# Kernel optimization log

Hardware: AMD Instinct MI355X
Metric: run time of the kernel (lower is better)

## Reference

```python
import jax, jax.numpy as jnp
import numpy as np

N_HEADS = 32
N_KV_HEADS = 8
HEAD_DIM = 128


def setup_inputs() -> dict:
    key = jax.random.key(0)
    ks = jax.random.split(key, 7)
    B, S, D = 2, 2048, 4096
    scale = 0.02
    x = jax.random.normal(ks[0], (B, S, D), dtype=jnp.float32)
    wq = jax.random.normal(ks[1], (D, D), dtype=jnp.float32) * scale
    wk = jax.random.normal(ks[2], (N_KV_HEADS * HEAD_DIM, D), dtype=jnp.float32) * scale
    wv = jax.random.normal(ks[3], (N_KV_HEADS * HEAD_DIM, D), dtype=jnp.float32) * scale
    wo = jax.random.normal(ks[4], (D, D), dtype=jnp.float32) * scale
    # RoPE frequencies: theta = 10000^{-2i/d}, angles = pos * theta
    inv_freq = 1.0 / (10000.0 ** (jnp.arange(0, HEAD_DIM, 2, dtype=jnp.float32) / HEAD_DIM))
    angles = jnp.arange(S, dtype=jnp.float32)[:, None] * inv_freq[None, :]  # (S, HEAD_DIM//2)
    freqs_cos = jnp.cos(angles)
    freqs_sin = jnp.sin(angles)
    # causal additive mask (0 on/below diagonal, -inf above)
    neg_inf = jnp.finfo(jnp.float32).min
    mask = jnp.where(jnp.triu(jnp.ones((S, S), dtype=bool), k=1), neg_inf, 0.0)[None, None]
    return {"x": x, "wq": wq, "wk": wk, "wv": wv, "wo": wo,
            "freqs_cos": freqs_cos, "freqs_sin": freqs_sin, "mask": mask,
            "start_pos": 0}


def _apply_rope(t, cos, sin):
    # t: (B, S, H, D); cos/sin: (S, D//2) -> broadcast (1, S, 1, D//2)
    b, s, h, d = t.shape
    tr = t.reshape(b, s, h, d // 2, 2)
    te, to = tr[..., 0], tr[..., 1]
    c = cos[None, :, None, :]
    si = sin[None, :, None, :]
    out = jnp.stack([te * c - to * si, te * si + to * c], axis=-1)
    return out.reshape(b, s, h, d)


def reference(x, wq, wk, wv, wo, freqs_cos, freqs_sin, mask, start_pos):
    b, s, d = x.shape
    n_rep = N_HEADS // N_KV_HEADS
    xq = (x @ wq.T).reshape(b, s, N_HEADS, HEAD_DIM)
    xk = (x @ wk.T).reshape(b, s, N_KV_HEADS, HEAD_DIM)
    xv = (x @ wv.T).reshape(b, s, N_KV_HEADS, HEAD_DIM)
    xq = _apply_rope(xq, freqs_cos, freqs_sin)
    xk = _apply_rope(xk, freqs_cos, freqs_sin)
    # repeat_kv: (B, S, Hkv, D) -> (B, S, Hkv*n_rep, D)
    keys = jnp.broadcast_to(xk[:, :, :, None, :], (b, s, N_KV_HEADS, n_rep, HEAD_DIM)).reshape(b, s, N_HEADS, HEAD_DIM)
    values = jnp.broadcast_to(xv[:, :, :, None, :], (b, s, N_KV_HEADS, n_rep, HEAD_DIM)).reshape(b, s, N_HEADS, HEAD_DIM)
    q = xq.transpose(0, 2, 1, 3)       # (B, H, S, D)
    k = keys.transpose(0, 2, 1, 3)
    v = values.transpose(0, 2, 1, 3)
    scores = jnp.einsum("bhqd,bhkd->bhqk", q, k) / np.sqrt(HEAD_DIM).astype(np.float32)
    scores = scores + mask
    probs = jax.nn.softmax(scores.astype(jnp.float32), axis=-1).astype(q.dtype)
    out = jnp.einsum("bhqk,bhkd->bhqd", probs, v)
    out = out.transpose(0, 2, 1, 3).reshape(b, s, N_HEADS * HEAD_DIM)
    return out @ wo.T
```

## Files before the change

### kernel.cpp

```cpp
#include <hip/hip_runtime.h>
#include <cstdint>
#include <cstddef>

#define B_  2
#define S_  2048
#define D_  4096
#define NH  32
#define NKV 8
#define HD  128

typedef unsigned short u16;
typedef unsigned int   u32;
typedef __attribute__((ext_vector_type(8))) short short8;
typedef __attribute__((ext_vector_type(4))) float f32x4;

__device__ __forceinline__ u16 f2bf(float f) {
  u32 u = __float_as_uint(f);
  u32 r = (u + 0x7FFFu + ((u >> 16) & 1u)) >> 16;
  return (u16)r;
}
__device__ __forceinline__ float bf2f(u32 lo16) {
  return __uint_as_float(lo16 << 16);
}
__device__ __forceinline__ u32 cvtpk_bf16(float lo, float hi) {
  u32 r;
  asm("v_cvt_pk_bf16_f32 %0, %1, %2" : "=v"(r) : "v"(lo), "v"(hi));
  return r;
}
__device__ __forceinline__ void load_lds16(const void* g, void* lds) {
  __builtin_amdgcn_global_load_lds(
      (const __attribute__((address_space(1))) u32*)g,
      (__attribute__((address_space(3))) u32*)lds, 16, 0, 0);
}

__global__ __launch_bounds__(256) void cvt_all(
    const float* __restrict__ x, const float* __restrict__ wq,
    const float* __restrict__ wk, const float* __restrict__ wv,
    const float* __restrict__ wo, u16* __restrict__ Xb, u16* __restrict__ Wqb,
    u16* __restrict__ Wkb, u16* __restrict__ Wvb, u16* __restrict__ Wob) {
  long i = (long)blockIdx.x * 256 + threadIdx.x;
  const float* src; u16* dst; long off;
  if (i < 2097152L)      { src = x;  dst = Xb;  off = i; }
  else if (i < 4194304L) { src = wq; dst = Wqb; off = i - 2097152L; }
  else if (i < 4718592L) { src = wk; dst = Wkb; off = i - 4194304L; }
  else if (i < 5242880L) { src = wv; dst = Wvb; off = i - 4718592L; }
  else                   { src = wo; dst = Wob; off = i - 5242880L; }
  const float4* s = (const float4*)src + off * 2;
  float4 a = s[0], b = s[1];
  uint4 o;
  o.x = (u32)f2bf(a.x) | ((u32)f2bf(a.y) << 16);
  o.y = (u32)f2bf(a.z) | ((u32)f2bf(a.w) << 16);
  o.z = (u32)f2bf(b.x) | ((u32)f2bf(b.y) << 16);
  o.w = (u32)f2bf(b.z) | ((u32)f2bf(b.w) << 16);
  *((uint4*)dst + off) = o;
}

template <int MODE, bool ROPE>
__global__ __launch_bounds__(512, 2)
void gemm256(const u16* __restrict__ A, const u16* __restrict__ Bw,
             void* __restrict__ Cout, int M, int N, int K, int Hh,
             const float* __restrict__ fc, const float* __restrict__ fs) {
  const int tid = threadIdx.x, lid = tid & 63, w = tid >> 6;
  const int lr = lid & 15, lg = lid >> 4;
  const int wm = w >> 2, wn = w & 3;

  int lin = blockIdx.y * gridDim.x + blockIdx.x;
  int bm, bn;
  if (gridDim.x == 16 && gridDim.y == 16) {
    int xcd = lin & 7, idx = lin >> 3;
    bm = ((xcd & 3) * 4 + (idx >> 3)) * 256;
    bn = ((xcd >> 2) * 8 + (idx & 7)) * 256;
  } else {
    bm = blockIdx.y * 256;
    bn = blockIdx.x * 256;
  }

  __shared__ __align__(16) u16 Al[2][2][8192];
  __shared__ __align__(16) u16 Bl[2][2][8192];

  f32x4 acc[8][4];
#pragma unroll
  for (int i = 0; i < 8; ++i)
#pragma unroll
    for (int j = 0; j < 4; ++j) acc[i][j] = (f32x4){0.f, 0.f, 0.f, 0.f};

#define STG_A(B2, KS, K0)                                                       \
  do {                                                                          \
    _Pragma("unroll")                                                           \
    for (int j_ = 0; j_ < 2; ++j_) {                                            \
      int c_ = j_ * 512 + tid;                                                  \
      int r_ = c_ >> 2, cb_ = c_ & 3;                                           \
      int s_ = (cb_ ^ (r_ >> 1)) & 3;                                           \
      load_lds16(A + (size_t)(bm + r_) * K + (K0) + (KS) * 32 + s_ * 8,         \
                 &Al[B2][KS][c_ * 8]);                                          \
    }                                                                           \
  } while (0)
#define STG_B(B2, KS, K0)                                                       \
  do {                                                                          \
    _Pragma("unroll")                                                           \
    for (int j_ = 0; j_ < 2; ++j_) {                                            \
      int c_ = j_ * 512 + tid;                                                  \
      int r_ = c_ >> 2, cb_ = c_ & 3;                                           \
      int s_ = (cb_ ^ (r_ >> 1)) & 3;                                           \
      load_lds16(Bw + (size_t)(bn + r_) * K + (K0) + (KS) * 32 + s_ * 8,        \
                 &Bl[B2][KS][c_ * 8]);                                          \
    }                                                                           \
  } while (0)

  const int nt = K >> 6;
  STG_A(0, 0, 0); STG_B(0, 0, 0); STG_A(0, 1, 0); STG_B(0, 1, 0);
  STG_A(1, 0, 64); STG_B(1, 0, 64);
  asm volatile("s_waitcnt vmcnt(8)" ::: "memory");
  __builtin_amdgcn_s_barrier();

  for (int t = 0; t < nt; ++t) {
    const int buf = t & 1, bufN = buf ^ 1;
    const int k1 = (t + 1) << 6, k2 = (t + 2) << 6;
    const bool pf1 = (t + 1 < nt), pf2 = (t + 2 < nt);
    short8 a[4], bfr[4];

#pragma unroll
    for (int ni = 0; ni < 4; ++ni) {
      int r = wn * 64 + ni * 16 + lr;
      bfr[ni] = *(const short8*)&Bl[buf][0][r * 32 + ((lg ^ (r >> 1)) & 3) * 8];
    }
#pragma unroll
    for (int mi = 0; mi < 4; ++mi) {
      int r = wm * 128 + mi * 16 + lr;
      a[mi] = *(const short8*)&Al[buf][0][r * 32 + ((lg ^ (r >> 1)) & 3) * 8];
    }
    if (pf1) STG_A(bufN, 1, k1);
    __builtin_amdgcn_s_barrier();
    __builtin_amdgcn_s_setprio(1);
#pragma unroll
    for (int mi = 0; mi < 4; ++mi)
#pragma unroll
      for (int ni = 0; ni < 4; ++ni)
        acc[mi][ni] = __builtin_amdgcn_mfma_f32_16x16x32_bf16(a[mi], bfr[ni], acc[mi][ni], 0, 0, 0);
    __builtin_amdgcn_s_setprio(0);

#pragma unroll
    for (int mi = 0; mi < 4; ++mi) {
      int r = wm * 128 + (mi + 4) * 16 + lr;
      a[mi] = *(const short8*)&Al[buf][0][r * 32 + ((lg ^ (r >> 1)) & 3) * 8];
    }
    if (pf1) STG_B(bufN, 1, k1);
    __builtin_amdgcn_s_barrier();
    __builtin_amdgcn_s_setprio(1);
#pragma unroll
    for (int mi = 0; mi < 4; ++mi)
#pragma unroll
      for (int ni = 0; ni < 4; ++ni)
        acc[mi + 4][ni] = __builtin_amdgcn_mfma_f32_16x16x32_bf16(a[mi], bfr[ni], acc[mi + 4][ni], 0, 0, 0);
    __builtin_amdgcn_s_setprio(0);

    if (pf1) asm volatile("s_waitcnt vmcnt(8)" ::: "memory");
    else     asm volatile("s_waitcnt vmcnt(0)" ::: "memory");
    __builtin_amdgcn_s_barrier();

#pragma unroll
    for (int ni = 0; ni < 4; ++ni) {
      int r = wn * 64 + ni * 16 + lr;
      bfr[ni] = *(const short8*)&Bl[buf][1][r * 32 + ((lg ^ (r >> 1)) & 3) * 8];
    }
#pragma unroll
    for (int mi = 0; mi < 4; ++mi) {
      int r = wm * 128 + mi * 16 + lr;
      a[mi] = *(const short8*)&Al[buf][1][r * 32 + ((lg ^ (r >> 1)) & 3) * 8];
    }
    if (pf2) STG_A(buf, 0, k2);
    __builtin_amdgcn_s_barrier();
    __builtin_amdgcn_s_setprio(1);
#pragma unroll
    for (int mi = 0; mi < 4; ++mi)
#pragma unroll
      for (int ni = 0; ni < 4; ++ni)
        acc[mi][ni] = __builtin_amdgcn_mfma_f32_16x16x32_bf16(a[mi], bfr[ni], acc[mi][ni], 0, 0, 0);
    __builtin_amdgcn_s_setprio(0);

#pragma unroll
    for (int mi = 0; mi < 4; ++mi) {
      int r = wm * 128 + (mi + 4) * 16 + lr;
      a[mi] = *(const short8*)&Al[buf][1][r * 32 + ((lg ^ (r >> 1)) & 3) * 8];
    }
    if (pf2) STG_B(buf, 0, k2);
    __builtin_amdgcn_s_barrier();
    __builtin_amdgcn_s_setprio(1);
#pragma unroll
    for (int mi = 0; mi < 4; ++mi)
#pragma unroll
      for (int ni = 0; ni < 4; ++ni)
        acc[mi + 4][ni] = __builtin_amdgcn_mfma_f32_16x16x32_bf16(a[mi], bfr[ni], acc[mi + 4][ni], 0, 0, 0);
    __builtin_amdgcn_s_setprio(0);

    if (pf1) {
      if (pf2) asm volatile("s_waitcnt vmcnt(8)" ::: "memory");
      else     asm volatile("s_waitcnt vmcnt(4)" ::: "memory");
      __builtin_amdgcn_s_barrier();
    }
  }
#undef STG_A
#undef STG_B

#pragma unroll
  for (int mi = 0; mi < 8; ++mi)
#pragma unroll
    for (int ni = 0; ni < 4; ++ni)
#pragma unroll
      for (int v = 0; v < 4; ++v) {
        int m = bm + wm * 128 + mi * 16 + lg * 4 + v;
        int n = bn + wn * 64 + ni * 16 + lr;
        float val = acc[mi][ni][v];
        if (ROPE) {
          int srow = m & (S_ - 1);
          int j = (n & (HD - 1)) >> 1;
          float c = fc[(size_t)srow * 64 + j];
          float s = fs[(size_t)srow * 64 + j];
          float partner = __shfl_xor(val, 1);
          val = (n & 1) ? (val * c + partner * s) : (val * c - partner * s);
        }
        if (MODE == 0) {
          ((float*)Cout)[(size_t)m * N + n] = val;
        } else if (MODE == 1) {
          int b = m >> 11, s = m & (S_ - 1), hh = n >> 7, d = n & (HD - 1);
          ((u16*)Cout)[(((size_t)(b * Hh + hh)) * S_ + s) * HD + d] = f2bf(val);
        } else {
          int b = m >> 11, s = m & (S_ - 1), hh = n >> 7, d = n & (HD - 1);
          ((u16*)Cout)[(((size_t)(b * Hh + hh)) * HD + d) * S_ + s] = f2bf(val);
        }
      }
}

__global__ __launch_bounds__(256)
void gemm_kv(const u16* __restrict__ Xb, const u16* __restrict__ Wk,
             const u16* __restrict__ Wv, u16* __restrict__ Kr, u16* __restrict__ Vt,
             const float* __restrict__ fc, const float* __restrict__ fs) {
  const int tid = threadIdx.x;
  const int lid = tid & 63, w = tid >> 6;
  const int lr = lid & 15, lg = lid >> 4;
  const int wm = w >> 1, wn = w & 1;
  const int zz = blockIdx.z;
  const u16* Bw = zz ? Wv : Wk;
  const int K = D_, N = NKV * HD;

  const int gx = gridDim.x;
  const int nwg = gx * gridDim.y;
  const int lin = blockIdx.y * gx + blockIdx.x;
  const int cpx = nwg >> 3;
  const int lin2 = (lin & 7) * cpx + (lin >> 3);
  const int bm = (lin2 / gx) * 128, bn = (lin2 % gx) * 128;

  __shared__ __align__(16) u16 Al[128 * 64];
  __shared__ __align__(16) u16 Bl[128 * 64];
  f32x4 acc[4][4];
#pragma unroll
  for (int i = 0; i < 4; ++i)
#pragma unroll
    for (int j = 0; j < 4; ++j) acc[i][j] = (f32x4){0.f, 0.f, 0.f, 0.f};

  for (int k0 = 0; k0 < K; k0 += 64) {
    __syncthreads();
#pragma unroll
    for (int i = 0; i < 4; ++i) {
      int c = i * 256 + tid;
      int row = c >> 3, cb = c & 7;
      int cbs = (cb ^ row) & 7;
      load_lds16(Xb + (size_t)(bm + row) * K + k0 + cbs * 8, &Al[c * 8]);
    }
#pragma unroll
    for (int i = 0; i < 4; ++i) {
      int c = i * 256 + tid;
      int row = c >> 3, cb = c & 7;
      int cbs = (cb ^ row) & 7;
      load_lds16(Bw + (size_t)(bn + row) * K + k0 + cbs * 8, &Bl[c * 8]);
    }
    __syncthreads();
#pragma unroll
    for (int ks = 0; ks < 2; ++ks) {
      short8 af[4], bf[4];
#pragma unroll
      for (int mi = 0; mi < 4; ++mi) {
        int row = wm * 64 + mi * 16 + lr;
        af[mi] = *(const short8*)&Al[row * 64 + (((ks * 4 + lg) ^ row) & 7) * 8];
      }
#pragma unroll
      for (int ni = 0; ni < 4; ++ni) {
        int row = wn * 64 + ni * 16 + lr;
        bf[ni] = *(const short8*)&Bl[row * 64 + (((ks * 4 + lg) ^ row) & 7) * 8];
      }
#pragma unroll
      for (int mi = 0; mi < 4; ++mi)
#pragma unroll
        for (int ni = 0; ni < 4; ++ni)
          acc[mi][ni] = __builtin_amdgcn_mfma_f32_16x16x32_bf16(af[mi], bf[ni], acc[mi][ni], 0, 0, 0);
    }
  }
#pragma unroll
  for (int mi = 0; mi < 4; ++mi)
#pragma unroll
    for (int ni = 0; ni < 4; ++ni)
#pragma unroll
      for (int v = 0; v < 4; ++v) {
        int m = bm + wm * 64 + mi * 16 + lg * 4 + v;
        int n = bn + wn * 64 + ni * 16 + lr;
        float val = acc[mi][ni][v];
        int b = m >> 11, s = m & (S_ - 1), hh = n >> 7, d = n & (HD - 1);
        if (zz == 0) {
          int j = d >> 1;
          float c = fc[(size_t)s * 64 + j];
          float sn = fs[(size_t)s * 64 + j];
          float partner = __shfl_xor(val, 1);
          val = (n & 1) ? (val * c + partner * sn) : (val * c - partner * sn);
          Kr[(((size_t)(b * NKV + hh)) * S_ + s) * HD + d] = f2bf(val);
        } else {
          Vt[(((size_t)(b * NKV + hh)) * HD + d) * S_ + s] = f2bf(val);
        }
      }
}

__global__ __launch_bounds__(512, 4)
void attn_k(const u16* __restrict__ Qr, const u16* __restrict__ Kr,
            const u16* __restrict__ Vt, u16* __restrict__ Ao) {
  const int xp = blockIdx.x, h = blockIdx.y, b = blockIdx.z;
  const int kvh = h >> 2;
  const int tid = threadIdx.x, lid = tid & 63, w = tid >> 6;
  const int lr = lid & 15, lg = lid >> 4;
  __shared__ __align__(16) u16 Kl[2][64 * 128];
  __shared__ __align__(16) u16 Vl[2][128 * 64];
  __shared__ __align__(16) u32 Plw[8 * 512];

  const size_t qbase = ((size_t)(b * NH + h)) * S_ * HD;
  const size_t kbase = ((size_t)(b * NKV + kvh)) * S_ * HD;
  const size_t vbase = ((size_t)(b * NKV + kvh)) * HD * S_;
  const float scl = 0.08838834764831845f * 1.44269504088896340f;
  const int pb = w * 512 + lr * 32;
  const int qx = 4 * (lr & 7);

#define STAGE(BUF, KT)                                                              \
  do {                                                                              \
    _Pragma("unroll")                                                               \
    for (int i_ = 0; i_ < 2; ++i_) {                                                \
      int c_ = i_ * 512 + tid;                                                      \
      int row_ = c_ >> 4, cb_ = c_ & 15;                                            \
      int cbs_ = (cb_ & 8) | ((cb_ ^ row_) & 7);                                    \
      load_lds16(&Kr[kbase + (size_t)((KT) + row_) * HD + cbs_ * 8],                \
                 &Kl[BUF][(i_ * 512 + w * 64) * 8]);                                \
    }                                                                               \
    _Pragma("unroll")                                                               \
    for (int i_ = 0; i_ < 2; ++i_) {                                                \
      int c_ = i_ * 512 + tid;                                                      \
      int d_ = c_ >> 3, cb_ = c_ & 7;                                               \
      int cbs_ = (cb_ ^ d_) & 7;                                                    \
      load_lds16(&Vt[vbase + (size_t)d_ * S_ + (KT) + cbs_ * 8],                    \
                 &Vl[BUF][(i_ * 512 + w * 64) * 8]);                                \
    }                                                                               \
  } while (0)

  for (int part = 0; part < 2; ++part) {
    const int qi = part ? xp : (15 - xp);
    const int qb = qi * 128;
    const int ntiles = qi * 2 + 2;
    const int q_abs = qb + w * 16 + lr;

    short8 qf[4];
#pragma unroll
    for (int ks = 0; ks < 4; ++ks)
      qf[ks] = *(const short8*)&Qr[qbase + (size_t)q_abs * HD + ks * 32 + lg * 8];

    float m2 = -3.0e38f, osum = 0.f;
    f32x4 oacc[8];
#pragma unroll
    for (int nd = 0; nd < 8; ++nd) oacc[nd] = (f32x4){0.f, 0.f, 0.f, 0.f};

    STAGE(0, 0);
    __syncthreads();
    int cur = 0;

    for (int t = 0; t < ntiles; ++t) {
      const int kt = t * 64;
      if (t + 1 < ntiles) STAGE(cur ^ 1, kt + 64);

      f32x4 sc[4];
#pragma unroll
      for (int ni = 0; ni < 4; ++ni) sc[ni] = (f32x4){0.f, 0.f, 0.f, 0.f};
      __builtin_amdgcn_s_setprio(1);
#pragma unroll
      for (int ks = 0; ks < 4; ++ks) {
#pragma unroll
        for (int ni = 0; ni < 4; ++ni) {
          int row = ni * 16 + lr;
          int ch = ks * 4 + lg;
          int chs = (ch & 8) | ((ch ^ row) & 7);
          short8 kf = *(const short8*)&Kl[cur][row * 128 + chs * 8];
          sc[ni] = __builtin_amdgcn_mfma_f32_16x16x32_bf16(kf, qf[ks], sc[ni], 0, 0, 0);
        }
      }
      __builtin_amdgcn_s_setprio(0);

      const bool edge = (kt + 64 > qb);
      float mx = -3.0e38f;
#pragma unroll
      for (int ni = 0; ni < 4; ++ni)
#pragma unroll
        for (int v = 0; v < 4; ++v) {
          float s = sc[ni][v] * scl;
          int kv = kt + ni * 16 + lg * 4 + v;
          if (edge && kv > q_abs) s = -3.0e38f;
          sc[ni][v] = s;
          mx = fmaxf(mx, s);
        }
      mx = fmaxf(mx, __shfl_xor(mx, 16));
      mx = fmaxf(mx, __shfl_xor(mx, 32));

      if (__any(mx > m2 + 8.0f)) {
        float mnew = fmaxf(m2, mx);
        float fr = exp2f(m2 - mnew);
        m2 = mnew;
        osum *= fr;
#pragma unroll
        for (int nd = 0; nd < 8; ++nd) oacc[nd] *= fr;
      }

      float ps = 0.f;
#pragma unroll
      for (int ni = 0; ni < 4; ++ni) {
#pragma unroll
        for (int p = 0; p < 2; ++p) {
          float e0 = exp2f(sc[ni][2 * p] - m2);
          float e1 = exp2f(sc[ni][2 * p + 1] - m2);
          ps += e0 + e1;
          Plw[pb + ((8 * ni + 2 * lg + p) ^ qx)] = cvtpk_bf16(e0, e1);
        }
      }
      osum += ps;

      asm volatile("s_waitcnt lgkmcnt(0)" ::: "memory");
      __builtin_amdgcn_sched_barrier(0);

      __builtin_amdgcn_s_setprio(1);
#pragma unroll
      for (int ks = 0; ks < 2; ++ks) {
        short8 pfk = *(const short8*)&Plw[pb + ((16 * ks + 4 * lg) ^ qx)];
#pragma unroll
        for (int nd = 0; nd < 8; ++nd) {
          int rowv = nd * 16 + lr;
          int ch = ks * 4 + lg;
          short8 vf = *(const short8*)&Vl[cur][rowv * 64 + ((ch ^ rowv) & 7) * 8];
          oacc[nd] = __builtin_amdgcn_mfma_f32_16x16x32_bf16(vf, pfk, oacc[nd], 0, 0, 0);
        }
      }
      __builtin_amdgcn_s_setprio(0);
      __syncthreads();
      cur ^= 1;
    }

    float os = osum;
    os += __shfl_xor(os, 16);
    os += __shfl_xor(os, 32);
    const float inv = 1.0f / os;
    const size_t orow = ((size_t)(b * S_ + q_abs)) * D_ + h * HD;
    u32* AoW = (u32*)Ao;
#pragma unroll
    for (int nd = 0; nd < 8; ++nd) {
#pragma unroll
      for (int p = 0; p < 2; ++p) {
        u32 pk = cvtpk_bf16(oacc[nd][2 * p] * inv, oacc[nd][2 * p + 1] * inv);
        AoW[(orow + nd * 16 + lg * 4 + 2 * p) >> 1] = pk;
      }
    }
  }
#undef STAGE
}

extern "C" void kernel_launch(void* const* d_in, const int* in_sizes, int n_in,
                              void* d_out, int out_size, void* d_ws, size_t ws_size,
                              hipStream_t stream) {
  const float* x  = (const float*)d_in[0];
  const float* wq = (const float*)d_in[1];
  const float* wk = (const float*)d_in[2];
  const float* wv = (const float*)d_in[3];
  const float* wo = (const float*)d_in[4];
  const float* fc = (const float*)d_in[5];
  const float* fs = (const float*)d_in[6];

  const size_t SZ_X  = (size_t)B_ * S_ * D_ * 2;
  const size_t SZ_WQ = (size_t)D_ * D_ * 2;
  const size_t SZ_WK = (size_t)NKV * HD * D_ * 2;
  char* ws = (char*)d_ws;
  u16* Xb  = (u16*)(ws);
  u16* Wqb = (u16*)(ws + SZ_X);
  u16* Wkb = (u16*)(ws + SZ_X + SZ_WQ);
  u16* Wvb = (u16*)(ws + SZ_X + SZ_WQ + SZ_WK);
  u16* Wob = (u16*)(ws + SZ_X + SZ_WQ + 2 * SZ_WK);
  u16* Qr  = (u16*)(ws + SZ_X + 2 * SZ_WQ + 2 * SZ_WK);
  u16* Kr  = (u16*)(ws + 2 * SZ_X + 2 * SZ_WQ + 2 * SZ_WK);
  u16* Vt  = (u16*)(ws + 2 * SZ_X + 2 * SZ_WQ + 3 * SZ_WK);
  u16* Ao  = (u16*)(ws + 2 * SZ_X + 2 * SZ_WQ + 4 * SZ_WK);
  const size_t NEEDED = 3 * SZ_X + 2 * SZ_WQ + 4 * SZ_WK;
  if (ws_size < NEEDED) return;

  cvt_all<<<28672, 256, 0, stream>>>(x, wq, wk, wv, wo, Xb, Wqb, Wkb, Wvb, Wob);

  gemm256<1, true><<<dim3(16, 16), 512, 0, stream>>>(
      Xb, Wqb, Qr, B_ * S_, D_, D_, NH, fc, fs);
  gemm_kv<<<dim3(8, 32, 2), 256, 0, stream>>>(Xb, Wkb, Wvb, Kr, Vt, fc, fs);

  attn_k<<<dim3(8, NH, B_), 512, 0, stream>>>(Qr, Kr, Vt, Ao);

  gemm256<0, false><<<dim3(16, 16), 512, 0, stream>>>(
      Ao, Wob, d_out, B_ * S_, D_, D_, 0, nullptr, nullptr);
}
```

Measured before the change: 522.8 us.

## Keep softmax probabilities in registers via permuted V layout, fold scale into Q

The V projection now writes V^T with a permuted sequence order inside each 32-column group. That order matches the register layout of the score MFMA output, so the bf16-packed probabilities can feed the PV MFMA directly from registers instead of going through an LDS scratch buffer. The softmax scale and log2e factor are folded into the Q projection epilogue, which removes a per-element multiply in the attention inner loop. The causal mask is applied only on edge tiles, and the max reduction is written as a tree. This removes LDS traffic, a wait on lgkmcnt and a sched barrier per tile, but it relies on the permutation exactly matching the MFMA operand layout.

```diff
diff --git a/kernel.cpp b/kernel.cpp
--- a/kernel.cpp
+++ b/kernel.cpp
@@ -13,6 +13,7 @@
 typedef unsigned int   u32;
 typedef __attribute__((ext_vector_type(8))) short short8;
 typedef __attribute__((ext_vector_type(4))) float f32x4;
+typedef __attribute__((ext_vector_type(4))) u32   u32x4;
 
 __device__ __forceinline__ u16 f2bf(float f) {
   u32 u = __float_as_uint(f);
@@ -26,6 +27,9 @@
   u32 r;
   asm("v_cvt_pk_bf16_f32 %0, %1, %2" : "=v"(r) : "v"(lo), "v"(hi));
   return r;
+}
+__device__ __forceinline__ short8 u32x4_to_short8(u32x4 v) {
+  union { u32x4 a; short8 b; } u; u.a = v; return u.b;
 }
 __device__ __forceinline__ void load_lds16(const void* g, void* lds) {
   __builtin_amdgcn_global_load_lds(
@@ -218,6 +222,7 @@
           float s = fs[(size_t)srow * 64 + j];
           float partner = __shfl_xor(val, 1);
           val = (n & 1) ? (val * c + partner * s) : (val * c - partner * s);
+          val *= (0.08838834764831845f * 1.44269504088896340f);
         }
         if (MODE == 0) {
           ((float*)Cout)[(size_t)m * N + n] = val;
@@ -241,7 +246,7 @@
   const int wm = w >> 1, wn = w & 1;
   const int zz = blockIdx.z;
   const u16* Bw = zz ? Wv : Wk;
-  const int K = D_, N = NKV * HD;
+  const int K = D_;
 
   const int gx = gridDim.x;
   const int nwg = gx * gridDim.y;
@@ -313,7 +318,9 @@
           val = (n & 1) ? (val * c + partner * sn) : (val * c - partner * sn);
           Kr[(((size_t)(b * NKV + hh)) * S_ + s) * HD + d] = f2bf(val);
         } else {
-          Vt[(((size_t)(b * NKV + hh)) * HD + d) * S_ + s] = f2bf(val);
+          int x = s & 31;
+          int sp = (s & ~31) | (((x >> 2) & 3) * 8 + ((x >> 4) & 1) * 4 + (x & 3));
+          Vt[(((size_t)(b * NKV + hh)) * HD + d) * S_ + sp] = f2bf(val);
         }
       }
 }
@@ -327,14 +334,10 @@
   const int lr = lid & 15, lg = lid >> 4;
   __shared__ __align__(16) u16 Kl[2][64 * 128];
   __shared__ __align__(16) u16 Vl[2][128 * 64];
-  __shared__ __align__(16) u32 Plw[8 * 512];
 
   const size_t qbase = ((size_t)(b * NH + h)) * S_ * HD;
   const size_t kbase = ((size_t)(b * NKV + kvh)) * S_ * HD;
   const size_t vbase = ((size_t)(b * NKV + kvh)) * HD * S_;
-  const float scl = 0.08838834764831845f * 1.44269504088896340f;
-  const int pb = w * 512 + lr * 32;
-  const int qx = 4 * (lr & 7);
 
 #define STAGE(BUF, KT)                                                              \
   do {                                                                              \
@@ -398,17 +401,20 @@
       __builtin_amdgcn_s_setprio(0);
 
       const bool edge = (kt + 64 > qb);
-      float mx = -3.0e38f;
-#pragma unroll
-      for (int ni = 0; ni < 4; ++ni)
-#pragma unroll
-        for (int v = 0; v < 4; ++v) {
-          float s = sc[ni][v] * scl;
-          int kv = kt + ni * 16 + lg * 4 + v;
-          if (edge && kv > q_abs) s = -3.0e38f;
-          sc[ni][v] = s;
-          mx = fmaxf(mx, s);
-        }
+      if (edge) {
+#pragma unroll
+        for (int ni = 0; ni < 4; ++ni)
+#pragma unroll
+          for (int v = 0; v < 4; ++v) {
+            int kv = kt + ni * 16 + lg * 4 + v;
+            if (kv > q_abs) sc[ni][v] = -3.0e38f;
+          }
+      }
+      float mab = fmaxf(fmaxf(fmaxf(sc[0][0], sc[0][1]), fmaxf(sc[0][2], sc[0][3])),
+                        fmaxf(fmaxf(sc[1][0], sc[1][1]), fmaxf(sc[1][2], sc[1][3])));
+      float mcd = fmaxf(fmaxf(fmaxf(sc[2][0], sc[2][1]), fmaxf(sc[2][2], sc[2][3])),
+                        fmaxf(fmaxf(sc[3][0], sc[3][1]), fmaxf(sc[3][2], sc[3][3])));
+      float mx = fmaxf(mab, mcd);
       mx = fmaxf(mx, __shfl_xor(mx, 16));
       mx = fmaxf(mx, __shfl_xor(mx, 32));
 
@@ -421,6 +427,7 @@
         for (int nd = 0; nd < 8; ++nd) oacc[nd] *= fr;
       }
 
+      u32x4 pw0, pw1;
       float ps = 0.f;
 #pragma unroll
       for (int ni = 0; ni < 4; ++ni) {
@@ -429,18 +436,19 @@
           float e0 = exp2f(sc[ni][2 * p] - m2);
           float e1 = exp2f(sc[ni][2 * p + 1] - m2);
           ps += e0 + e1;
-          Plw[pb + ((8 * ni + 2 * lg + p) ^ qx)] = cvtpk_bf16(e0, e1);
+          u32 pk = cvtpk_bf16(e0, e1);
+          if (ni < 2) pw0[(ni & 1) * 2 + p] = pk;
+          else        pw1[(ni & 1) * 2 + p] = pk;
         }
       }
       osum += ps;
-
-      asm volatile("s_waitcnt lgkmcnt(0)" ::: "memory");
-      __builtin_amdgcn_sched_barrier(0);
+      const short8 pf0 = u32x4_to_short8(pw0);
+      const short8 pf1 = u32x4_to_short8(pw1);
 
       __builtin_amdgcn_s_setprio(1);
 #pragma unroll
       for (int ks = 0; ks < 2; ++ks) {
-        short8 pfk = *(const short8*)&Plw[pb + ((16 * ks + 4 * lg) ^ qx)];
+        const short8 pfk = ks ? pf1 : pf0;
 #pragma unroll
         for (int nd = 0; nd < 8; ++nd) {
           int rowv = nd * 16 + lr;
```

Result: faster. 507.8 us (-2.9%).
